# Optimization experiments

Hardware: AMD Instinct MI355X
Metric: run time of the kernel (lower is better)

Reference implementation:

```python
import jax, jax.numpy as jnp
import numpy as np

DIM = 64; NH = 4; WS = (2, 7, 7); FRAMES = 8
# torch code uses head_dim = dim // num_heads for BOTH attentions' scale
SCALE = (DIM // NH) ** -0.5

def _rel_pos_index(ws):
    coords = np.stack(np.meshgrid(np.arange(ws[0]), np.arange(ws[1]), np.arange(ws[2]), indexing='ij'))
    cf = coords.reshape(3, -1)
    rc = (cf[:, :, None] - cf[:, None, :]).transpose(1, 2, 0)
    rc[:, :, 0] += ws[0] - 1; rc[:, :, 1] += ws[1] - 1; rc[:, :, 2] += ws[2] - 1
    rc[:, :, 0] *= (2 * ws[1] - 1) * (2 * ws[2] - 1)
    rc[:, :, 1] *= 2 * ws[2] - 1
    return jnp.asarray(rc.sum(-1))

REL_S = _rel_pos_index(WS)              # (98, 98)
REL_T = _rel_pos_index((FRAMES, 1, 1))  # (8, 8)

def _ln(x, g, b, eps=1e-5):
    m = x.mean(-1, keepdims=True)
    v = ((x - m) ** 2).mean(-1, keepdims=True)
    return (x - m) * jax.lax.rsqrt(v + eps) * g + b

def _conv3d(x, w, b):
    y = jax.lax.conv_general_dilated(x, w, (1, 1, 1), [(1, 1)] * 3,
                                     dimension_numbers=('NCDHW', 'OIDHW', 'NCDHW'))
    return y + b[None, :, None, None, None]

def setup_inputs():
    key = jax.random.key(0)
    ks = jax.random.split(key, 16)
    B, D, H, W, C = 2, 8, 112, 112, DIM
    C2 = C // 2
    n = lambda i, shape: jax.random.normal(ks[i], shape, jnp.float32) * 0.02
    return dict(
        x=jax.random.normal(ks[0], (B, D, H, W, C), jnp.float32),
        mask_matrix=jnp.zeros((1, 98, 98), jnp.float32),
        g1=jnp.ones((C,), jnp.float32), b1=jnp.zeros((C,), jnp.float32),
        rpb_s=n(1, ((2*WS[0]-1)*(2*WS[1]-1)*(2*WS[2]-1), NH)),
        qkv_w_s=n(2, (C, 3*C)), qkv_b_s=jnp.zeros((3*C,), jnp.float32),
        proj_w_s=n(3, (C, C)), proj_b_s=jnp.zeros((C,), jnp.float32),
        rpb_t=n(4, (2*FRAMES-1, NH)),
        qkv_w_t=n(5, (C, 3*C2)), qkv_b_t=jnp.zeros((3*C2,), jnp.float32),
        proj_w_t=n(6, (C2, C)), proj_b_t=jnp.zeros((C,), jnp.float32),
        g2=jnp.ones((C,), jnp.float32), b2=jnp.zeros((C,), jnp.float32),
        p1c1_w=n(7, (C2, C2, 3, 3, 3)), p1c1_b=jnp.zeros((C2,), jnp.float32),
        p1c2_w=n(8, (C2, C2, 3, 3, 3)), p1c2_b=jnp.zeros((C2,), jnp.float32),
        p2c1_w=n(9, (C2, C2, 3, 3, 3)), p2c1_b=jnp.zeros((C2,), jnp.float32),
        p2c2_w=n(10, (C2, C2, 3, 3, 3)), p2c2_b=jnp.zeros((C2,), jnp.float32),
    )

def reference(x, mask_matrix, g1, b1, rpb_s, qkv_w_s, qkv_b_s, proj_w_s, proj_b_s,
              rpb_t, qkv_w_t, qkv_b_t, proj_w_t, proj_b_t, g2, b2,
              p1c1_w, p1c1_b, p1c2_w, p1c2_b, p2c1_w, p2c1_b, p2c2_w, p2c2_b):
    B, D, H, W, C = x.shape
    C2 = C // 2
    wd, wh, ww = WS
    N = wd * wh * ww
    shortcut = x
    h = _ln(x, g1, b1)
    # ---- space attention over (2,7,7) windows (shift=0, H/W/D divisible -> no pad/roll/mask) ----
    xw = h.reshape(B, D // wd, wd, H // wh, wh, W // ww, ww, C)
    xw = xw.transpose(0, 1, 3, 5, 2, 4, 6, 7).reshape(-1, N, C)  # (nW, N, C)
    nw = xw.shape[0]
    qkv = (xw @ qkv_w_s + qkv_b_s).reshape(nw, N, 3, NH, C // NH).transpose(2, 0, 3, 1, 4)
    q, k, v = qkv[0] * SCALE, qkv[1], qkv[2]
    attn = jnp.einsum('whnd,whmd->whnm', q, k)
    bias = rpb_s[REL_S.reshape(-1)].reshape(N, N, NH).transpose(2, 0, 1)
    attn = jax.nn.softmax(attn + bias[None], axis=-1)
    out = jnp.einsum('whnm,whmd->whnd', attn, v).transpose(0, 2, 1, 3).reshape(nw, N, C)
    out = out @ proj_w_s + proj_b_s
    space = out.reshape(B, D // wd, H // wh, W // ww, wd, wh, ww, C)
    space = space.transpose(0, 1, 4, 2, 5, 3, 6, 7).reshape(B, D, H, W, C)
    # ---- time attention over frames (qkv projects to C/2) ----
    xt = h.transpose(0, 2, 3, 1, 4).reshape(B * H * W, D, C)
    qkv_t = (xt @ qkv_w_t + qkv_b_t).reshape(-1, D, 3, NH, C2 // NH).transpose(2, 0, 3, 1, 4)
    qt, kt, vt = qkv_t[0] * SCALE, qkv_t[1], qkv_t[2]
    at = jnp.einsum('bhnd,bhmd->bhnm', qt, kt)
    bias_t = rpb_t[REL_T.reshape(-1)].reshape(D, D, NH).transpose(2, 0, 1)
    at = jax.nn.softmax(at + bias_t[None], axis=-1)
    ot = jnp.einsum('bhnm,bhmd->bhnd', at, vt).transpose(0, 2, 1, 3).reshape(-1, D, C2)
    ot = ot @ proj_w_t + proj_b_t  # (B*H*W, D, C)
    time = ot.reshape(B, H, W, D, C).transpose(0, 3, 1, 2, 4)
    x = shortcut + time + space
    # ---- GRFFNet conv FFN ----
    h2 = _ln(x, g2, b2).transpose(0, 4, 1, 2, 3)  # (B,C,D,H,W)
    x1, x2 = h2[:, :C2], h2[:, C2:]
    y1 = x1 + _conv3d(jax.nn.leaky_relu(_conv3d(x1, p1c1_w, p1c1_b)), p1c2_w, p1c2_b)
    x2 = x2 + y1
    y2 = x2 + _conv3d(jax.nn.leaky_relu(_conv3d(x2, p2c1_w, p2c1_b)), p2c2_w, p2c2_b)
    y = jnp.concatenate([y1, y2], axis=1).transpose(0, 2, 3, 4, 1)
    return x + y
```

## Files before the change

kernel.cpp:

```cpp
#include <hip/hip_runtime.h>
#include <hip/hip_bf16.h>

typedef unsigned short u16;
typedef unsigned int u32;
typedef __attribute__((ext_vector_type(8))) short s16x8;
typedef __attribute__((ext_vector_type(4))) float f32x4;

__device__ __forceinline__ u16 f2b(float v) {
  u32 bits = __float_as_uint(v);
  bits += 0x7fffu + ((bits >> 16) & 1u);
  return (u16)(bits >> 16);
}
__device__ __forceinline__ float b2f(u16 u) { return __uint_as_float(((u32)u) << 16); }
__device__ __forceinline__ float bflo(u32 w) { return __uint_as_float(w << 16); }
__device__ __forceinline__ float bfhi(u32 w) { return __uint_as_float(w & 0xffff0000u); }

__global__ __launch_bounds__(256) void k_ln(const float* __restrict__ x, const float* __restrict__ g,
    const float* __restrict__ b, float* __restrict__ hout, float* __restrict__ acc, u16* __restrict__ xb) {
  int token = blockIdx.x * 4 + (threadIdx.x >> 6);
  int lane = threadIdx.x & 63;
  long base = (long)token * 64 + lane;
  float v = x[base];
  float s = v;
#pragma unroll
  for (int o = 32; o; o >>= 1) s += __shfl_xor(s, o);
  float m = s * 0.015625f;
  float d = v - m;
  float q = d * d;
#pragma unroll
  for (int o = 32; o; o >>= 1) q += __shfl_xor(q, o);
  float r = rsqrtf(q * 0.015625f + 1e-5f);
  float hv = d * r * g[lane] + b[lane];
  hout[base] = hv;
  if (acc) acc[base] = v;
  if (xb && lane < 32) xb[(long)token * 32 + lane] = f2b(hv);
}

__global__ __launch_bounds__(256) void k_swprep(const float* __restrict__ qw, u16* __restrict__ swb) {
  int i = blockIdx.x * 256 + threadIdx.x;
  int kk = i & 31, q = i >> 5;
  int lm = q & 15, ksnt = q >> 4;
  int ks = ksnt & 1, nt = ksnt >> 1;
  swb[i] = f2b(qw[(ks * 32 + kk) * 192 + nt * 16 + lm]);
}

__global__ __launch_bounds__(256) void k_twprep(const float* __restrict__ qw, u16* __restrict__ twb) {
  int i = blockIdx.x * 256 + threadIdx.x;
  int kk = i & 31, q = i >> 5;
  int lm = q & 15, ksnt = q >> 4;
  int ks = ksnt & 1, nt = ksnt >> 1;
  twb[i] = f2b(qw[(ks * 32 + kk) * 96 + nt * 16 + lm]);
}

__global__ __launch_bounds__(256) void k_pwprep(const float* __restrict__ pw, u16* __restrict__ pwb) {
  int i = blockIdx.x * 256 + threadIdx.x;
  int r = i & 7, q = i >> 3;
  int col = q & 15; q >>= 4;
  int lk = q & 1; q >>= 1;
  int nt = q & 3, hd = q >> 2;
  pwb[i] = f2b(pw[(hd * 16 + lk * 8 + r) * 64 + nt * 16 + col]);
}

__global__ __launch_bounds__(256) void k_bprep(const float* __restrict__ rpb, float* __restrict__ Bt) {
  int i = blockIdx.x * 256 + threadIdx.x;
  int m = i % 112, q = i / 112;
  int n = q % 112, hd = q / 112;
  float v = -1e30f;
  if (n < 98 && m < 98) {
    int dzn = n / 49, rn = n % 49, hyn = rn / 7, wxn = rn % 7;
    int dzm = m / 49, rm = m % 49, hym = rm / 7, wxm = rm % 7;
    int idx = (dzn - dzm + 1) * 169 + (hyn - hym + 6) * 13 + (wxn - wxm + 6);
    v = rpb[idx * 4 + hd];
  }
  Bt[i] = v;
}

__global__ __launch_bounds__(256) void k_qkvs2(const float* __restrict__ h, const u16* __restrict__ swb,
    const float* __restrict__ qb, u16* __restrict__ Qg, u16* __restrict__ Kg, u16* __restrict__ Vg) {
  int l = threadIdx.x & 63, wv = threadIdx.x >> 6;
  int lm = l & 15, lk = l >> 4;
  long t0 = (long)blockIdx.x * 64 + wv * 16;
  const float* hp = h + (t0 + lm) * 64;
  s16x8 A[2];
#pragma unroll
  for (int ks = 0; ks < 2; ks++) {
    float4 x0 = *(const float4*)(hp + ks * 32 + lk * 8);
    float4 x1 = *(const float4*)(hp + ks * 32 + lk * 8 + 4);
    s16x8 a;
    a[0] = (short)f2b(x0.x); a[1] = (short)f2b(x0.y); a[2] = (short)f2b(x0.z); a[3] = (short)f2b(x0.w);
    a[4] = (short)f2b(x1.x); a[5] = (short)f2b(x1.y); a[6] = (short)f2b(x1.z); a[7] = (short)f2b(x1.w);
    A[ks] = a;
  }
  f32x4 C[12];
#pragma unroll
  for (int nt = 0; nt < 12; nt++) C[nt] = (f32x4){0.f, 0.f, 0.f, 0.f};
#pragma unroll
  for (int ks = 0; ks < 2; ks++) {
#pragma unroll
    for (int nt = 0; nt < 12; nt++) {
      s16x8 B = *(const s16x8*)&swb[((nt * 2 + ks) * 16 + lm) * 32 + lk * 8];
      C[nt] = __builtin_amdgcn_mfma_f32_16x16x32_bf16(A[ks], B, C[nt], 0, 0, 0);
    }
  }
  float qbv[12];
#pragma unroll
  for (int nt = 0; nt < 12; nt++) qbv[nt] = qb[nt * 16 + lm];
#pragma unroll
  for (int r = 0; r < 4; r++) {
    long t = t0 + lk * 4 + r;
    int b = (int)(t / 100352); int r1 = (int)(t - (long)b * 100352);
    int d = r1 / 12544; int r2 = r1 - d * 12544;
    int hy = r2 / 112, wx = r2 - hy * 112;
    int d0 = d >> 1, dz = d & 1, h0 = hy / 7, oy = hy - h0 * 7, w0 = wx / 7, ox = wx - w0 * 7;
    int wi = ((b * 4 + d0) * 16 + h0) * 16 + w0;
    int n = dz * 49 + oy * 7 + ox;
    long base = (long)(wi * 4) * 1568 + n * 16 + lm;
#pragma unroll
    for (int nt = 0; nt < 12; nt++) {
      int part = nt >> 2, hd = nt & 3;
      float v = C[nt][r] + qbv[nt];
      long o = base + hd * 1568;
      if (part == 0) Qg[o] = f2b(v * 0.25f);
      else if (part == 1) Kg[o] = f2b(v);
      else Vg[o] = f2b(v);
    }
  }
}

__global__ __launch_bounds__(512) void k_sattn3(const u16* __restrict__ Qg, const u16* __restrict__ Kg,
    const u16* __restrict__ Vg, const float* __restrict__ Bt, const u16* __restrict__ pwb,
    const float* __restrict__ pb, float* __restrict__ accg) {
  __shared__ __align__(16) u16 sQ[112 * 24];
  __shared__ __align__(16) u16 sK[112 * 24];
  __shared__ __align__(16) u16 sVt[16 * 136];
  __shared__ __align__(16) u16 sP[112 * 120 + 32];
  __shared__ __align__(16) u16 sO[112 * 24];
  int tid = threadIdx.x;
  int wi = blockIdx.x;
  int l = tid & 63, wv = tid >> 6;
  int lm = l & 15, lk = l >> 4;

  for (int i = tid; i < 336; i += 512) { sQ[2352 + i] = 0; sK[2352 + i] = 0; }
  for (int i = tid; i < 224; i += 512) { sVt[(i / 14) * 136 + 98 + (i % 14)] = 0; }

  int mt = wv;
  bool act = mt < 7;
  int baserow = mt * 16 + lk * 4;
  f32x4 po[4];
#pragma unroll
  for (int b = 0; b < 4; b++) po[b] = (f32x4){0.f, 0.f, 0.f, 0.f};

  for (int hd = 0; hd < 4; hd++) {
    __syncthreads();
    long base = (long)(wi * 4 + hd) * 1568;
    const u32* qp = (const u32*)(Qg + base);
    const u32* kp = (const u32*)(Kg + base);
    const u32* vp = (const u32*)(Vg + base);
    for (int i = tid; i < 784; i += 512) {
      u32 v = qp[i];
      int n = i >> 3, j2 = (i & 7) * 2;
      *(u32*)&sQ[n * 24 + j2] = v;
    }
    for (int i = tid; i < 784; i += 512) {
      u32 v = kp[i];
      int n = i >> 3, j2 = (i & 7) * 2;
      *(u32*)&sK[n * 24 + j2] = v;
    }
    for (int i = tid; i < 784; i += 512) {
      u32 v = vp[i];
      int n = i >> 3, j2 = (i & 7) * 2;
      sVt[j2 * 136 + n] = (u16)(v & 0xffffu);
      sVt[(j2 + 1) * 136 + n] = (u16)(v >> 16);
    }
    __syncthreads();
    if (!act) continue;

    s16x8 Aq = {};
    if (lk < 2) Aq = *(const s16x8*)&sQ[(mt * 16 + lm) * 24 + lk * 8];
    f32x4 S[7];
#pragma unroll
    for (int nt = 0; nt < 7; nt++) {
      s16x8 Bk = {};
      if (lk < 2) Bk = *(const s16x8*)&sK[(nt * 16 + lm) * 24 + lk * 8];
      S[nt] = __builtin_amdgcn_mfma_f32_16x16x32_bf16(Aq, Bk, (f32x4){0.f, 0.f, 0.f, 0.f}, 0, 0, 0);
    }
    const float* bt = Bt + hd * 12544 + baserow * 112 + lm;
    float mx0 = -3e38f, mx1 = -3e38f, mx2 = -3e38f, mx3 = -3e38f;
#pragma unroll
    for (int nt = 0; nt < 7; nt++) {
      S[nt][0] += bt[nt * 16];
      S[nt][1] += bt[112 + nt * 16];
      S[nt][2] += bt[224 + nt * 16];
      S[nt][3] += bt[336 + nt * 16];
      mx0 = fmaxf(mx0, S[nt][0]); mx1 = fmaxf(mx1, S[nt][1]);
      mx2 = fmaxf(mx2, S[nt][2]); mx3 = fmaxf(mx3, S[nt][3]);
    }
#pragma unroll
    for (int off = 1; off < 16; off <<= 1) {
      mx0 = fmaxf(mx0, __shfl_xor(mx0, off));
      mx1 = fmaxf(mx1, __shfl_xor(mx1, off));
      mx2 = fmaxf(mx2, __shfl_xor(mx2, off));
      mx3 = fmaxf(mx3, __shfl_xor(mx3, off));
    }
    float s0 = 0.f, s1 = 0.f, s2 = 0.f, s3 = 0.f;
#pragma unroll
    for (int nt = 0; nt < 7; nt++) {
      S[nt][0] = __expf(S[nt][0] - mx0); s0 += S[nt][0];
      S[nt][1] = __expf(S[nt][1] - mx1); s1 += S[nt][1];
      S[nt][2] = __expf(S[nt][2] - mx2); s2 += S[nt][2];
      S[nt][3] = __expf(S[nt][3] - mx3); s3 += S[nt][3];
    }
#pragma unroll
    for (int off = 1; off < 16; off <<= 1) {
      s0 += __shfl_xor(s0, off); s1 += __shfl_xor(s1, off);
      s2 += __shfl_xor(s2, off); s3 += __shfl_xor(s3, off);
    }
    float i0 = 1.f / s0, i1 = 1.f / s1, i2 = 1.f / s2, i3 = 1.f / s3;
#pragma unroll
    for (int nt = 0; nt < 7; nt++) {
      int c = nt * 16 + lm;
      sP[(baserow + 0) * 120 + c] = f2b(S[nt][0] * i0);
      sP[(baserow + 1) * 120 + c] = f2b(S[nt][1] * i1);
      sP[(baserow + 2) * 120 + c] = f2b(S[nt][2] * i2);
      sP[(baserow + 3) * 120 + c] = f2b(S[nt][3] * i3);
    }
    int rowoff = (mt * 16 + lm) * 120;
    f32x4 pv = (f32x4){0.f, 0.f, 0.f, 0.f};
#pragma unroll
    for (int ks = 0; ks < 3; ks++) {
      s16x8 Ap = *(const s16x8*)&sP[rowoff + ks * 32 + lk * 8];
      s16x8 Bv = *(const s16x8*)&sVt[lm * 136 + ks * 32 + lk * 8];
      pv = __builtin_amdgcn_mfma_f32_16x16x32_bf16(Ap, Bv, pv, 0, 0, 0);
    }
    {
      s16x8 Ap = {}, Bv = {};
      if (lk < 2) {
        Ap = *(const s16x8*)&sP[rowoff + 96 + lk * 8];
        Bv = *(const s16x8*)&sVt[lm * 136 + 96 + lk * 8];
      }
      pv = __builtin_amdgcn_mfma_f32_16x16x32_bf16(Ap, Bv, pv, 0, 0, 0);
    }
#pragma unroll
    for (int r = 0; r < 4; r++) sO[(baserow + r) * 24 + lm] = f2b(pv[r]);
    s16x8 Ao = {};
    if (lk < 2) Ao = *(const s16x8*)&sO[(mt * 16 + lm) * 24 + lk * 8];
#pragma unroll
    for (int nt = 0; nt < 4; nt++) {
      s16x8 Bw = {};
      if (lk < 2) Bw = *(const s16x8*)&pwb[((((hd * 4 + nt) * 2 + lk) * 16 + lm) * 8)];
      po[nt] = __builtin_amdgcn_mfma_f32_16x16x32_bf16(Ao, Bw, po[nt], 0, 0, 0);
    }
  }
  if (act) {
    int b = wi >> 10, d0 = (wi >> 8) & 3, h0 = (wi >> 4) & 15, w0 = wi & 15;
    float pbv[4];
#pragma unroll
    for (int nt = 0; nt < 4; nt++) pbv[nt] = pb[nt * 16 + lm];
#pragma unroll
    for (int r = 0; r < 4; r++) {
      int n = mt * 16 + lk * 4 + r;
      if (n >= 98) continue;
      int dz = n / 49, rr = n - dz * 49, oy = rr / 7, ox = rr - oy * 7;
      long p = ((long)(b * 8 + d0 * 2 + dz) * 112 + (h0 * 7 + oy)) * 112 + (w0 * 7 + ox);
      float* ap = accg + p * 64;
#pragma unroll
      for (int nt = 0; nt < 4; nt++) {
        int col = nt * 16 + lm;
        ap[col] += po[nt][r] + pbv[nt];
      }
    }
  }
}

__global__ __launch_bounds__(256) void k_qkvt(const float* __restrict__ h, const u16* __restrict__ twb,
    const float* __restrict__ qb, u16* __restrict__ T) {
  int l = threadIdx.x & 63, wv = threadIdx.x >> 6;
  int lm = l & 15, lk = l >> 4;
  long t0 = (long)blockIdx.x * 64 + wv * 16;
  const float* hp = h + (t0 + lm) * 64;
  s16x8 A[2];
#pragma unroll
  for (int ks = 0; ks < 2; ks++) {
    float4 x0 = *(const float4*)(hp + ks * 32 + lk * 8);
    float4 x1 = *(const float4*)(hp + ks * 32 + lk * 8 + 4);
    s16x8 a;
    a[0] = (short)f2b(x0.x); a[1] = (short)f2b(x0.y); a[2] = (short)f2b(x0.z); a[3] = (short)f2b(x0.w);
    a[4] = (short)f2b(x1.x); a[5] = (short)f2b(x1.y); a[6] = (short)f2b(x1.z); a[7] = (short)f2b(x1.w);
    A[ks] = a;
  }
  f32x4 C[6];
#pragma unroll
  for (int nt = 0; nt < 6; nt++) C[nt] = (f32x4){0.f, 0.f, 0.f, 0.f};
#pragma unroll
  for (int ks = 0; ks < 2; ks++) {
#pragma unroll
    for (int nt = 0; nt < 6; nt++) {
      s16x8 B = *(const s16x8*)&twb[((nt * 2 + ks) * 16 + lm) * 32 + lk * 8];
      C[nt] = __builtin_amdgcn_mfma_f32_16x16x32_bf16(A[ks], B, C[nt], 0, 0, 0);
    }
  }
  float qbv[6];
#pragma unroll
  for (int nt = 0; nt < 6; nt++) qbv[nt] = qb[nt * 16 + lm];
#pragma unroll
  for (int r = 0; r < 4; r++) {
    long t = t0 + lk * 4 + r;
    int bb = (int)(t / 100352); int r1 = (int)(t - (long)bb * 100352);
    int d = r1 / 12544; int rr = r1 - d * 12544;
    long sidx = ((long)(bb * 12544 + rr) * 8 + d) * 96;
#pragma unroll
    for (int nt = 0; nt < 6; nt++) {
      int ch = nt * 16 + lm;
      float v = C[nt][r] + qbv[nt];
      if (nt < 2) v *= 0.25f;
      T[sidx + ch] = f2b(v);
    }
  }
}

__global__ __launch_bounds__(256) void k_tattn2(const u16* __restrict__ T, const float* __restrict__ rpbt,
    const float* __restrict__ pw, const float* __restrict__ pb, float* __restrict__ acc) {
  __shared__ float sm[4][1064];
  int wv = threadIdx.x >> 6, lane = threadIdx.x & 63;
  int s = blockIdx.x * 4 + wv;
  int b = s / 12544, rr = s - b * 12544;
  float* sq = sm[wv];
  float* o = sq + 800;
  const u32* Tp = (const u32*)(T + (long)s * 768);
  for (int i = lane; i < 192; i += 64) {
    u32 lo = Tp[i * 2], hi = Tp[i * 2 + 1];
    int d = i / 24, base = (i - d * 24) * 4;
    float* dst = sq + d * 100 + base;
    dst[0] = bflo(lo); dst[1] = bfhi(lo); dst[2] = bflo(hi); dst[3] = bfhi(hi);
  }
  __syncthreads();
  if (lane < 32) {
    int hd = lane >> 3, n = lane & 7;
    const float* qr = sq + n * 100 + hd * 8;
    float p[8];
    float mx = -3e38f;
#pragma unroll
    for (int m = 0; m < 8; m++) {
      const float* kr = sq + m * 100 + 32 + hd * 8;
      float sc = 0.f;
#pragma unroll
      for (int e = 0; e < 8; e++) sc += qr[e] * kr[e];
      sc += rpbt[(n - m + 7) * 4 + hd];
      p[m] = sc; mx = fmaxf(mx, sc);
    }
    float sum = 0.f;
#pragma unroll
    for (int m = 0; m < 8; m++) { p[m] = __expf(p[m] - mx); sum += p[m]; }
    float inv = 1.f / sum;
#pragma unroll
    for (int j = 0; j < 8; j++) {
      float oj = 0.f;
#pragma unroll
      for (int m = 0; m < 8; m++) oj += p[m] * sq[m * 100 + 64 + hd * 8 + j];
      o[n * 33 + hd * 8 + j] = oj * inv;
    }
  }
  __syncthreads();
  float a[8];
  float pbc = pb[lane];
#pragma unroll
  for (int n = 0; n < 8; n++) a[n] = pbc;
  for (int k = 0; k < 32; k++) {
    float w = pw[k * 64 + lane];
#pragma unroll
    for (int n = 0; n < 8; n++) a[n] += o[n * 33 + k] * w;
  }
  long base = ((long)b * 100352 + rr) * 64 + lane;
#pragma unroll
  for (int n = 0; n < 8; n++) acc[base + (long)n * 802816] += a[n];
}

__global__ __launch_bounds__(256) void k_wprep(const float* __restrict__ w0, const float* __restrict__ w1,
    const float* __restrict__ w2, const float* __restrict__ w3, u16* __restrict__ WB) {
  int c = blockIdx.y;
  int i = blockIdx.x * 256 + threadIdx.x;
  const float* src = c == 0 ? w0 : c == 1 ? w1 : c == 2 ? w2 : w3;
  int co = i / 864, rem = i - co * 864, ci = rem / 27, kk = rem - ci * 27;
  WB[c * 27648 + kk * 1024 + co * 32 + ci] = f2b(src[i]);
}

__global__ __launch_bounds__(64) void k_convm(const u16* __restrict__ in, const u16* __restrict__ wb,
    const float* __restrict__ bias, int mode,
    const float* __restrict__ hbuf, const float* __restrict__ accb,
    float* __restrict__ dout, float* __restrict__ x2f, u16* __restrict__ outb) {
  int row = blockIdx.x;
  int hh = row % 112, bz = row / 112;
  int d = bz & 7, bb = bz >> 3;
  long prow = (long)row * 112;
  int l = threadIdx.x, lm = l & 15, lk = l >> 4;
  f32x4 acc[7][2];
#pragma unroll
  for (int t = 0; t < 7; t++) { acc[t][0] = (f32x4){0.f,0.f,0.f,0.f}; acc[t][1] = (f32x4){0.f,0.f,0.f,0.f}; }
  for (int kd = 0; kd < 3; kd++) {
    int zd = d + kd - 1;
    if (zd < 0 || zd > 7) continue;
    for (int kh = 0; kh < 3; kh++) {
      int yy = hh + kh - 1;
      if (yy < 0 || yy > 111) continue;
      const u16* ip = in + ((long)((bb * 8 + zd) * 112 + yy)) * 112 * 32;
      int kkb = kd * 9 + kh * 3;
      s16x8 B0[3], B1[3];
#pragma unroll
      for (int kw = 0; kw < 3; kw++) {
        const u16* wp = wb + (kkb + kw) * 1024 + lk * 8;
        B0[kw] = *(const s16x8*)(wp + lm * 32);
        B1[kw] = *(const s16x8*)(wp + (16 + lm) * 32);
      }
#pragma unroll
      for (int t = 0; t < 7; t++) {
#pragma unroll
        for (int kw = 0; kw < 3; kw++) {
          int w = t * 16 + lm + kw - 1;
          s16x8 A = {};
          if ((unsigned)w < 112u) A = *(const s16x8*)(ip + (long)w * 32 + lk * 8);
          acc[t][0] = __builtin_amdgcn_mfma_f32_16x16x32_bf16(A, B0[kw], acc[t][0], 0, 0, 0);
          acc[t][1] = __builtin_amdgcn_mfma_f32_16x16x32_bf16(A, B1[kw], acc[t][1], 0, 0, 0);
        }
      }
    }
  }
  float b0 = bias[lm], b1 = bias[16 + lm];
#pragma unroll
  for (int t = 0; t < 7; t++) {
#pragma unroll
    for (int r = 0; r < 4; r++) {
      long pos = prow + t * 16 + lk * 4 + r;
      float v0 = acc[t][0][r] + b0;
      float v1 = acc[t][1][r] + b1;
      if (mode == 1) {
        v0 = v0 > 0.f ? v0 : 0.01f * v0;
        v1 = v1 > 0.f ? v1 : 0.01f * v1;
        outb[pos * 32 + lm] = f2b(v0);
        outb[pos * 32 + 16 + lm] = f2b(v1);
      } else if (mode == 2) {
        float y0 = v0 + hbuf[pos * 64 + lm];
        float y1v = v1 + hbuf[pos * 64 + 16 + lm];
        dout[pos * 64 + lm] = accb[pos * 64 + lm] + y0;
        dout[pos * 64 + 16 + lm] = accb[pos * 64 + 16 + lm] + y1v;
        float t0 = hbuf[pos * 64 + 32 + lm] + y0;
        float t1 = hbuf[pos * 64 + 48 + lm] + y1v;
        x2f[pos * 32 + lm] = t0;
        x2f[pos * 32 + 16 + lm] = t1;
        outb[pos * 32 + lm] = f2b(t0);
        outb[pos * 32 + 16 + lm] = f2b(t1);
      } else {
        float y0 = v0 + x2f[pos * 32 + lm];
        float y1v = v1 + x2f[pos * 32 + 16 + lm];
        dout[pos * 64 + 32 + lm] = accb[pos * 64 + 32 + lm] + y0;
        dout[pos * 64 + 48 + lm] = accb[pos * 64 + 48 + lm] + y1v;
      }
    }
  }
}

extern "C" void kernel_launch(void* const* d_in, const int* in_sizes, int n_in,
                              void* d_out, int out_size, void* d_ws, size_t ws_size,
                              hipStream_t stream) {
  const float* x        = (const float*)d_in[0];
  const float* g1       = (const float*)d_in[2];
  const float* b1       = (const float*)d_in[3];
  const float* rpb_s    = (const float*)d_in[4];
  const float* qkv_w_s  = (const float*)d_in[5];
  const float* qkv_b_s  = (const float*)d_in[6];
  const float* proj_w_s = (const float*)d_in[7];
  const float* proj_b_s = (const float*)d_in[8];
  const float* rpb_t    = (const float*)d_in[9];
  const float* qkv_w_t  = (const float*)d_in[10];
  const float* qkv_b_t  = (const float*)d_in[11];
  const float* proj_w_t = (const float*)d_in[12];
  const float* proj_b_t = (const float*)d_in[13];
  const float* g2       = (const float*)d_in[14];
  const float* b2       = (const float*)d_in[15];
  const float* c1w = (const float*)d_in[16];
  const float* c1b = (const float*)d_in[17];
  const float* c2w = (const float*)d_in[18];
  const float* c2b = (const float*)d_in[19];
  const float* c3w = (const float*)d_in[20];
  const float* c3b = (const float*)d_in[21];
  const float* c4w = (const float*)d_in[22];
  const float* c4b = (const float*)d_in[23];

  float* acc  = (float*)d_ws;
  float* hbuf = acc + 12845056;
  float* creg = hbuf + 12845056;
  u16* Qg = (u16*)creg;
  u16* Kg = Qg + 12845056;
  u16* Vg = Kg + 12845056;
  u16* Tt = (u16*)creg;
  u16* x1b = (u16*)creg;
  u16* t_b = x1b + 6422528;
  u16* x2b = t_b + 6422528;
  float* x2f = (float*)(x2b + 6422528);
  u16* WB = (u16*)(x2f + 6422528);
  float* dout = (float*)d_out;
  u16* pwb = (u16*)d_out;
  u16* twb = (u16*)d_out + 4096;
  u16* swb = (u16*)d_out + 10240;
  float* Bt = (float*)d_out + 11264;

  k_pwprep<<<16, 256, 0, stream>>>(proj_w_s, pwb);
  k_twprep<<<24, 256, 0, stream>>>(qkv_w_t, twb);
  k_swprep<<<48, 256, 0, stream>>>(qkv_w_s, swb);
  k_bprep<<<196, 256, 0, stream>>>(rpb_s, Bt);
  k_ln<<<50176, 256, 0, stream>>>(x, g1, b1, hbuf, acc, nullptr);
  k_qkvs2<<<3136, 256, 0, stream>>>(hbuf, swb, qkv_b_s, Qg, Kg, Vg);
  k_sattn3<<<2048, 512, 0, stream>>>(Qg, Kg, Vg, Bt, pwb, proj_b_s, acc);
  k_qkvt<<<3136, 256, 0, stream>>>(hbuf, twb, qkv_b_t, Tt);
  k_tattn2<<<6272, 256, 0, stream>>>(Tt, rpb_t, proj_w_t, proj_b_t, acc);
  k_wprep<<<dim3(108, 4), 256, 0, stream>>>(c1w, c2w, c3w, c4w, WB);
  k_ln<<<50176, 256, 0, stream>>>(acc, g2, b2, hbuf, nullptr, x1b);
  k_convm<<<1792, 64, 0, stream>>>(x1b, WB, c1b, 1, nullptr, nullptr, nullptr, nullptr, t_b);
  k_convm<<<1792, 64, 0, stream>>>(t_b, WB + 27648, c2b, 2, hbuf, acc, dout, x2f, x2b);
  k_convm<<<1792, 64, 0, stream>>>(x2b, WB + 2 * 27648, c3b, 1, nullptr, nullptr, nullptr, nullptr, t_b);
  k_convm<<<1792, 64, 0, stream>>>(t_b, WB + 3 * 27648, c4b, 4, nullptr, acc, dout, x2f, nullptr);
}
```

Measured before the change: 465.1 us.

## Fuse first LayerNorm with spatial and temporal QKV projections; split conv rows

Merges the four weight-prep kernels into one launch. Fuses the first LayerNorm, the copy of x into the residual accumulator, and both the spatial and temporal QKV projections into a single kernel, so the normalized activations never round-trip through a float buffer and x is read only once. The temporal QKV output now lives in the hbuf region instead of overlapping the spatial Q buffer. The conv kernel is split over two grid columns of up to four 16-wide tiles each, which doubles the block count and cuts per-block accumulator registers. The cost is more register pressure in the fused kernel and more redundant weight loads across the conv blocks.

```diff
diff --git a/kernel.cpp b/kernel.cpp
--- a/kernel.cpp
+++ b/kernel.cpp
@@ -16,7 +16,7 @@
 __device__ __forceinline__ float bfhi(u32 w) { return __uint_as_float(w & 0xffff0000u); }
 
 __global__ __launch_bounds__(256) void k_ln(const float* __restrict__ x, const float* __restrict__ g,
-    const float* __restrict__ b, float* __restrict__ hout, float* __restrict__ acc, u16* __restrict__ xb) {
+    const float* __restrict__ b, float* __restrict__ hout, u16* __restrict__ xb) {
   int token = blockIdx.x * 4 + (threadIdx.x >> 6);
   int lane = threadIdx.x & 63;
   long base = (long)token * 64 + lane;
@@ -32,68 +32,110 @@
   float r = rsqrtf(q * 0.015625f + 1e-5f);
   float hv = d * r * g[lane] + b[lane];
   hout[base] = hv;
-  if (acc) acc[base] = v;
-  if (xb && lane < 32) xb[(long)token * 32 + lane] = f2b(hv);
-}
-
-__global__ __launch_bounds__(256) void k_swprep(const float* __restrict__ qw, u16* __restrict__ swb) {
+  if (lane < 32) xb[(long)token * 32 + lane] = f2b(hv);
+}
+
+__global__ __launch_bounds__(256) void k_prep(const float* __restrict__ pw, u16* __restrict__ pwb,
+    const float* __restrict__ tqw, u16* __restrict__ twb,
+    const float* __restrict__ sqw, u16* __restrict__ swb,
+    const float* __restrict__ rpb, float* __restrict__ Bt) {
   int i = blockIdx.x * 256 + threadIdx.x;
-  int kk = i & 31, q = i >> 5;
-  int lm = q & 15, ksnt = q >> 4;
-  int ks = ksnt & 1, nt = ksnt >> 1;
-  swb[i] = f2b(qw[(ks * 32 + kk) * 192 + nt * 16 + lm]);
-}
-
-__global__ __launch_bounds__(256) void k_twprep(const float* __restrict__ qw, u16* __restrict__ twb) {
-  int i = blockIdx.x * 256 + threadIdx.x;
-  int kk = i & 31, q = i >> 5;
-  int lm = q & 15, ksnt = q >> 4;
-  int ks = ksnt & 1, nt = ksnt >> 1;
-  twb[i] = f2b(qw[(ks * 32 + kk) * 96 + nt * 16 + lm]);
-}
-
-__global__ __launch_bounds__(256) void k_pwprep(const float* __restrict__ pw, u16* __restrict__ pwb) {
-  int i = blockIdx.x * 256 + threadIdx.x;
-  int r = i & 7, q = i >> 3;
-  int col = q & 15; q >>= 4;
-  int lk = q & 1; q >>= 1;
-  int nt = q & 3, hd = q >> 2;
-  pwb[i] = f2b(pw[(hd * 16 + lk * 8 + r) * 64 + nt * 16 + col]);
-}
-
-__global__ __launch_bounds__(256) void k_bprep(const float* __restrict__ rpb, float* __restrict__ Bt) {
-  int i = blockIdx.x * 256 + threadIdx.x;
-  int m = i % 112, q = i / 112;
-  int n = q % 112, hd = q / 112;
-  float v = -1e30f;
-  if (n < 98 && m < 98) {
-    int dzn = n / 49, rn = n % 49, hyn = rn / 7, wxn = rn % 7;
-    int dzm = m / 49, rm = m % 49, hym = rm / 7, wxm = rm % 7;
-    int idx = (dzn - dzm + 1) * 169 + (hyn - hym + 6) * 13 + (wxn - wxm + 6);
-    v = rpb[idx * 4 + hd];
-  }
-  Bt[i] = v;
-}
-
-__global__ __launch_bounds__(256) void k_qkvs2(const float* __restrict__ h, const u16* __restrict__ swb,
-    const float* __restrict__ qb, u16* __restrict__ Qg, u16* __restrict__ Kg, u16* __restrict__ Vg) {
+  if (i < 4096) {
+    int r = i & 7, q = i >> 3;
+    int col = q & 15; q >>= 4;
+    int lk = q & 1; q >>= 1;
+    int nt = q & 3, hd = q >> 2;
+    pwb[i] = f2b(pw[(hd * 16 + lk * 8 + r) * 64 + nt * 16 + col]);
+  } else if (i < 10240) {
+    int j = i - 4096;
+    int kk = j & 31, q = j >> 5;
+    int lm = q & 15, ksnt = q >> 4;
+    int ks = ksnt & 1, nt = ksnt >> 1;
+    twb[j] = f2b(tqw[(ks * 32 + kk) * 96 + nt * 16 + lm]);
+  } else if (i < 22528) {
+    int j = i - 10240;
+    int kk = j & 31, q = j >> 5;
+    int lm = q & 15, ksnt = q >> 4;
+    int ks = ksnt & 1, nt = ksnt >> 1;
+    swb[j] = f2b(sqw[(ks * 32 + kk) * 192 + nt * 16 + lm]);
+  } else {
+    int j = i - 22528;
+    int m = j % 112, q = j / 112;
+    int n = q % 112, hd = q / 112;
+    float v = -1e30f;
+    if (n < 98 && m < 98) {
+      int dzn = n / 49, rn = n % 49, hyn = rn / 7, wxn = rn % 7;
+      int dzm = m / 49, rm = m % 49, hym = rm / 7, wxm = rm % 7;
+      int idx = (dzn - dzm + 1) * 169 + (hyn - hym + 6) * 13 + (wxn - wxm + 6);
+      v = rpb[idx * 4 + hd];
+    }
+    Bt[j] = v;
+  }
+}
+
+__global__ __launch_bounds__(256) void k_wprep(const float* __restrict__ w0, const float* __restrict__ w1,
+    const float* __restrict__ w2, const float* __restrict__ w3, u16* __restrict__ WB) {
+  int j = blockIdx.x * 256 + threadIdx.x;
+  int c = j / 27648, j2 = j - c * 27648;
+  const float* src = c == 0 ? w0 : c == 1 ? w1 : c == 2 ? w2 : w3;
+  int co = j2 / 864, rem = j2 - co * 864, ci = rem / 27, kk = rem - ci * 27;
+  WB[c * 27648 + kk * 1024 + co * 32 + ci] = f2b(src[j2]);
+}
+
+__global__ __launch_bounds__(256) void k_fused1(const float* __restrict__ x,
+    const float* __restrict__ g1, const float* __restrict__ b1,
+    const u16* __restrict__ swb, const float* __restrict__ sqb,
+    const u16* __restrict__ twb, const float* __restrict__ tqb,
+    float* __restrict__ acc, u16* __restrict__ Qg, u16* __restrict__ Kg,
+    u16* __restrict__ Vg, u16* __restrict__ T) {
   int l = threadIdx.x & 63, wv = threadIdx.x >> 6;
   int lm = l & 15, lk = l >> 4;
   long t0 = (long)blockIdx.x * 64 + wv * 16;
-  const float* hp = h + (t0 + lm) * 64;
+  long tok = t0 + lm;
+  const float* xp = x + tok * 64 + lk * 8;
+  float* ap = acc + tok * 64 + lk * 8;
+  float va[16];
+  float s = 0.f;
+#pragma unroll
+  for (int ks = 0; ks < 2; ks++) {
+    float4 a0 = *(const float4*)(xp + ks * 32);
+    float4 a1 = *(const float4*)(xp + ks * 32 + 4);
+    *(float4*)(ap + ks * 32) = a0;
+    *(float4*)(ap + ks * 32 + 4) = a1;
+    va[ks * 8 + 0] = a0.x; va[ks * 8 + 1] = a0.y; va[ks * 8 + 2] = a0.z; va[ks * 8 + 3] = a0.w;
+    va[ks * 8 + 4] = a1.x; va[ks * 8 + 5] = a1.y; va[ks * 8 + 6] = a1.z; va[ks * 8 + 7] = a1.w;
+    s += a0.x + a0.y + a0.z + a0.w + a1.x + a1.y + a1.z + a1.w;
+  }
+  s += __shfl_xor(s, 16); s += __shfl_xor(s, 32);
+  float m = s * 0.015625f;
+  float q = 0.f;
+#pragma unroll
+  for (int j = 0; j < 16; j++) { float d = va[j] - m; q += d * d; }
+  q += __shfl_xor(q, 16); q += __shfl_xor(q, 32);
+  float r = rsqrtf(q * 0.015625f + 1e-5f);
   s16x8 A[2];
 #pragma unroll
   for (int ks = 0; ks < 2; ks++) {
-    float4 x0 = *(const float4*)(hp + ks * 32 + lk * 8);
-    float4 x1 = *(const float4*)(hp + ks * 32 + lk * 8 + 4);
+    float4 g0 = *(const float4*)(g1 + ks * 32 + lk * 8);
+    float4 g4 = *(const float4*)(g1 + ks * 32 + lk * 8 + 4);
+    float4 c0 = *(const float4*)(b1 + ks * 32 + lk * 8);
+    float4 c4 = *(const float4*)(b1 + ks * 32 + lk * 8 + 4);
     s16x8 a;
-    a[0] = (short)f2b(x0.x); a[1] = (short)f2b(x0.y); a[2] = (short)f2b(x0.z); a[3] = (short)f2b(x0.w);
-    a[4] = (short)f2b(x1.x); a[5] = (short)f2b(x1.y); a[6] = (short)f2b(x1.z); a[7] = (short)f2b(x1.w);
+    a[0] = (short)f2b((va[ks * 8 + 0] - m) * r * g0.x + c0.x);
+    a[1] = (short)f2b((va[ks * 8 + 1] - m) * r * g0.y + c0.y);
+    a[2] = (short)f2b((va[ks * 8 + 2] - m) * r * g0.z + c0.z);
+    a[3] = (short)f2b((va[ks * 8 + 3] - m) * r * g0.w + c0.w);
+    a[4] = (short)f2b((va[ks * 8 + 4] - m) * r * g4.x + c4.x);
+    a[5] = (short)f2b((va[ks * 8 + 5] - m) * r * g4.y + c4.y);
+    a[6] = (short)f2b((va[ks * 8 + 6] - m) * r * g4.z + c4.z);
+    a[7] = (short)f2b((va[ks * 8 + 7] - m) * r * g4.w + c4.w);
     A[ks] = a;
   }
-  f32x4 C[12];
+  f32x4 C[12], D[6];
 #pragma unroll
   for (int nt = 0; nt < 12; nt++) C[nt] = (f32x4){0.f, 0.f, 0.f, 0.f};
+#pragma unroll
+  for (int nt = 0; nt < 6; nt++) D[nt] = (f32x4){0.f, 0.f, 0.f, 0.f};
 #pragma unroll
   for (int ks = 0; ks < 2; ks++) {
 #pragma unroll
@@ -101,28 +143,42 @@
       s16x8 B = *(const s16x8*)&swb[((nt * 2 + ks) * 16 + lm) * 32 + lk * 8];
       C[nt] = __builtin_amdgcn_mfma_f32_16x16x32_bf16(A[ks], B, C[nt], 0, 0, 0);
     }
-  }
-  float qbv[12];
-#pragma unroll
-  for (int nt = 0; nt < 12; nt++) qbv[nt] = qb[nt * 16 + lm];
-#pragma unroll
-  for (int r = 0; r < 4; r++) {
-    long t = t0 + lk * 4 + r;
+#pragma unroll
+    for (int nt = 0; nt < 6; nt++) {
+      s16x8 B = *(const s16x8*)&twb[((nt * 2 + ks) * 16 + lm) * 32 + lk * 8];
+      D[nt] = __builtin_amdgcn_mfma_f32_16x16x32_bf16(A[ks], B, D[nt], 0, 0, 0);
+    }
+  }
+  float sbv[12], tbv[6];
+#pragma unroll
+  for (int nt = 0; nt < 12; nt++) sbv[nt] = sqb[nt * 16 + lm];
+#pragma unroll
+  for (int nt = 0; nt < 6; nt++) tbv[nt] = tqb[nt * 16 + lm];
+#pragma unroll
+  for (int r4 = 0; r4 < 4; r4++) {
+    long t = t0 + lk * 4 + r4;
     int b = (int)(t / 100352); int r1 = (int)(t - (long)b * 100352);
     int d = r1 / 12544; int r2 = r1 - d * 12544;
     int hy = r2 / 112, wx = r2 - hy * 112;
     int d0 = d >> 1, dz = d & 1, h0 = hy / 7, oy = hy - h0 * 7, w0 = wx / 7, ox = wx - w0 * 7;
     int wi = ((b * 4 + d0) * 16 + h0) * 16 + w0;
     int n = dz * 49 + oy * 7 + ox;
-    long base = (long)(wi * 4) * 1568 + n * 16 + lm;
+    long sbase = (long)(wi * 4) * 1568 + n * 16 + lm;
 #pragma unroll
     for (int nt = 0; nt < 12; nt++) {
       int part = nt >> 2, hd = nt & 3;
-      float v = C[nt][r] + qbv[nt];
-      long o = base + hd * 1568;
+      float v = C[nt][r4] + sbv[nt];
+      long o = sbase + hd * 1568;
       if (part == 0) Qg[o] = f2b(v * 0.25f);
       else if (part == 1) Kg[o] = f2b(v);
       else Vg[o] = f2b(v);
+    }
+    long sidx = ((long)(b * 12544 + r2) * 8 + d) * 96;
+#pragma unroll
+    for (int nt = 0; nt < 6; nt++) {
+      float v = D[nt][r4] + tbv[nt];
+      if (nt < 2) v *= 0.25f;
+      T[sidx + nt * 16 + lm] = f2b(v);
     }
   }
 }
@@ -268,52 +324,6 @@
         int col = nt * 16 + lm;
         ap[col] += po[nt][r] + pbv[nt];
       }
-    }
-  }
-}
-
-__global__ __launch_bounds__(256) void k_qkvt(const float* __restrict__ h, const u16* __restrict__ twb,
-    const float* __restrict__ qb, u16* __restrict__ T) {
-  int l = threadIdx.x & 63, wv = threadIdx.x >> 6;
-  int lm = l & 15, lk = l >> 4;
-  long t0 = (long)blockIdx.x * 64 + wv * 16;
-  const float* hp = h + (t0 + lm) * 64;
-  s16x8 A[2];
-#pragma unroll
-  for (int ks = 0; ks < 2; ks++) {
-    float4 x0 = *(const float4*)(hp + ks * 32 + lk * 8);
-    float4 x1 = *(const float4*)(hp + ks * 32 + lk * 8 + 4);
-    s16x8 a;
-    a[0] = (short)f2b(x0.x); a[1] = (short)f2b(x0.y); a[2] = (short)f2b(x0.z); a[3] = (short)f2b(x0.w);
-    a[4] = (short)f2b(x1.x); a[5] = (short)f2b(x1.y); a[6] = (short)f2b(x1.z); a[7] = (short)f2b(x1.w);
-    A[ks] = a;
-  }
-  f32x4 C[6];
-#pragma unroll
-  for (int nt = 0; nt < 6; nt++) C[nt] = (f32x4){0.f, 0.f, 0.f, 0.f};
-#pragma unroll
-  for (int ks = 0; ks < 2; ks++) {
-#pragma unroll
-    for (int nt = 0; nt < 6; nt++) {
-      s16x8 B = *(const s16x8*)&twb[((nt * 2 + ks) * 16 + lm) * 32 + lk * 8];
-      C[nt] = __builtin_amdgcn_mfma_f32_16x16x32_bf16(A[ks], B, C[nt], 0, 0, 0);
-    }
-  }
-  float qbv[6];
-#pragma unroll
-  for (int nt = 0; nt < 6; nt++) qbv[nt] = qb[nt * 16 + lm];
-#pragma unroll
-  for (int r = 0; r < 4; r++) {
-    long t = t0 + lk * 4 + r;
-    int bb = (int)(t / 100352); int r1 = (int)(t - (long)bb * 100352);
-    int d = r1 / 12544; int rr = r1 - d * 12544;
-    long sidx = ((long)(bb * 12544 + rr) * 8 + d) * 96;
-#pragma unroll
-    for (int nt = 0; nt < 6; nt++) {
-      int ch = nt * 16 + lm;
-      float v = C[nt][r] + qbv[nt];
-      if (nt < 2) v *= 0.25f;
-      T[sidx + ch] = f2b(v);
     }
   }
 }
@@ -375,27 +385,19 @@
   for (int n = 0; n < 8; n++) acc[base + (long)n * 802816] += a[n];
 }
 
-__global__ __launch_bounds__(256) void k_wprep(const float* __restrict__ w0, const float* __restrict__ w1,
-    const float* __restrict__ w2, const float* __restrict__ w3, u16* __restrict__ WB) {
-  int c = blockIdx.y;
-  int i = blockIdx.x * 256 + threadIdx.x;
-  const float* src = c == 0 ? w0 : c == 1 ? w1 : c == 2 ? w2 : w3;
-  int co = i / 864, rem = i - co * 864, ci = rem / 27, kk = rem - ci * 27;
-  WB[c * 27648 + kk * 1024 + co * 32 + ci] = f2b(src[i]);
-}
-
 __global__ __launch_bounds__(64) void k_convm(const u16* __restrict__ in, const u16* __restrict__ wb,
     const float* __restrict__ bias, int mode,
     const float* __restrict__ hbuf, const float* __restrict__ accb,
     float* __restrict__ dout, float* __restrict__ x2f, u16* __restrict__ outb) {
   int row = blockIdx.x;
+  int tb = blockIdx.y * 4;
   int hh = row % 112, bz = row / 112;
   int d = bz & 7, bb = bz >> 3;
   long prow = (long)row * 112;
   int l = threadIdx.x, lm = l & 15, lk = l >> 4;
-  f32x4 acc[7][2];
-#pragma unroll
-  for (int t = 0; t < 7; t++) { acc[t][0] = (f32x4){0.f,0.f,0.f,0.f}; acc[t][1] = (f32x4){0.f,0.f,0.f,0.f}; }
+  f32x4 acc[4][2];
+#pragma unroll
+  for (int q = 0; q < 4; q++) { acc[q][0] = (f32x4){0.f,0.f,0.f,0.f}; acc[q][1] = (f32x4){0.f,0.f,0.f,0.f}; }
   for (int kd = 0; kd < 3; kd++) {
     int zd = d + kd - 1;
     if (zd < 0 || zd > 7) continue;
@@ -412,26 +414,30 @@
         B1[kw] = *(const s16x8*)(wp + (16 + lm) * 32);
       }
 #pragma unroll
-      for (int t = 0; t < 7; t++) {
+      for (int q = 0; q < 4; q++) {
+        int t = tb + q;
+        if (t > 6) continue;
 #pragma unroll
         for (int kw = 0; kw < 3; kw++) {
           int w = t * 16 + lm + kw - 1;
           s16x8 A = {};
           if ((unsigned)w < 112u) A = *(const s16x8*)(ip + (long)w * 32 + lk * 8);
-          acc[t][0] = __builtin_amdgcn_mfma_f32_16x16x32_bf16(A, B0[kw], acc[t][0], 0, 0, 0);
-          acc[t][1] = __builtin_amdgcn_mfma_f32_16x16x32_bf16(A, B1[kw], acc[t][1], 0, 0, 0);
+          acc[q][0] = __builtin_amdgcn_mfma_f32_16x16x32_bf16(A, B0[kw], acc[q][0], 0, 0, 0);
+          acc[q][1] = __builtin_amdgcn_mfma_f32_16x16x32_bf16(A, B1[kw], acc[q][1], 0, 0, 0);
         }
       }
     }
   }
   float b0 = bias[lm], b1 = bias[16 + lm];
 #pragma unroll
-  for (int t = 0; t < 7; t++) {
+  for (int q = 0; q < 4; q++) {
+    int t = tb + q;
+    if (t > 6) continue;
 #pragma unroll
     for (int r = 0; r < 4; r++) {
       long pos = prow + t * 16 + lk * 4 + r;
-      float v0 = acc[t][0][r] + b0;
-      float v1 = acc[t][1][r] + b1;
+      float v0 = acc[q][0][r] + b0;
+      float v1 = acc[q][1][r] + b1;
       if (mode == 1) {
         v0 = v0 > 0.f ? v0 : 0.01f * v0;
         v1 = v1 > 0.f ? v1 : 0.01f * v1;
@@ -491,7 +497,7 @@
   u16* Qg = (u16*)creg;
   u16* Kg = Qg + 12845056;
   u16* Vg = Kg + 12845056;
-  u16* Tt = (u16*)creg;
+  u16* Tt = (u16*)hbuf;
   u16* x1b = (u16*)creg;
   u16* t_b = x1b + 6422528;
   u16* x2b = t_b + 6422528;
@@ -503,19 +509,15 @@
   u16* swb = (u16*)d_out + 10240;
   float* Bt = (float*)d_out + 11264;
 
-  k_pwprep<<<16, 256, 0, stream>>>(proj_w_s, pwb);
-  k_twprep<<<24, 256, 0, stream>>>(qkv_w_t, twb);
-  k_swprep<<<48, 256, 0, stream>>>(qkv_w_s, swb);
-  k_bprep<<<196, 256, 0, stream>>>(rpb_s, Bt);
-  k_ln<<<50176, 256, 0, stream>>>(x, g1, b1, hbuf, acc, nullptr);
-  k_qkvs2<<<3136, 256, 0, stream>>>(hbuf, swb, qkv_b_s, Qg, Kg, Vg);
+  k_prep<<<284, 256, 0, stream>>>(proj_w_s, pwb, qkv_w_t, twb, qkv_w_s, swb, rpb_s, Bt);
+  k_fused1<<<3136, 256, 0, stream>>>(x, g1, b1, swb, qkv_b_s, twb, qkv_b_t,
+                                     acc, Qg, Kg, Vg, Tt);
   k_sattn3<<<2048, 512, 0, stream>>>(Qg, Kg, Vg, Bt, pwb, proj_b_s, acc);
-  k_qkvt<<<3136, 256, 0, stream>>>(hbuf, twb, qkv_b_t, Tt);
+  k_wprep<<<432, 256, 0, stream>>>(c1w, c2w, c3w, c4w, WB);
   k_tattn2<<<6272, 256, 0, stream>>>(Tt, rpb_t, proj_w_t, proj_b_t, acc);
-  k_wprep<<<dim3(108, 4), 256, 0, stream>>>(c1w, c2w, c3w, c4w, WB);
-  k_ln<<<50176, 256, 0, stream>>>(acc, g2, b2, hbuf, nullptr, x1b);
-  k_convm<<<1792, 64, 0, stream>>>(x1b, WB, c1b, 1, nullptr, nullptr, nullptr, nullptr, t_b);
-  k_convm<<<1792, 64, 0, stream>>>(t_b, WB + 27648, c2b, 2, hbuf, acc, dout, x2f, x2b);
-  k_convm<<<1792, 64, 0, stream>>>(x2b, WB + 2 * 27648, c3b, 1, nullptr, nullptr, nullptr, nullptr, t_b);
-  k_convm<<<1792, 64, 0, stream>>>(t_b, WB + 3 * 27648, c4b, 4, nullptr, acc, dout, x2f, nullptr);
-}
+  k_ln<<<50176, 256, 0, stream>>>(acc, g2, b2, hbuf, x1b);
+  k_convm<<<dim3(1792, 2), 64, 0, stream>>>(x1b, WB, c1b, 1, nullptr, nullptr, nullptr, nullptr, t_b);
+  k_convm<<<dim3(1792, 2), 64, 0, stream>>>(t_b, WB + 27648, c2b, 2, hbuf, acc, dout, x2f, x2b);
+  k_convm<<<dim3(1792, 2), 64, 0, stream>>>(x2b, WB + 2 * 27648, c3b, 1, nullptr, nullptr, nullptr, nullptr, t_b);
+  k_convm<<<dim3(1792, 2), 64, 0, stream>>>(t_b, WB + 3 * 27648, c4b, 4, nullptr, acc, dout, x2f, nullptr);
+}
```

New measurement: 485.6 us. 4.4% more time.
